# Kernel optimization log

Hardware: AMD Instinct MI355X
Metric: run time of the kernel (lower is better)

Reference implementation:

```python
import jax, jax.numpy as jnp
import numpy as np

CH = 512
GROUPS = 32
EPS = 1e-6


def setup_inputs() -> dict:
    key = jax.random.key(0)
    ks = jax.random.split(key, 12)
    b, c, h, w = 4, CH, 64, 64
    std = 1.0 / np.sqrt(c)
    return {
        "x": jax.random.normal(ks[0], (b, c, h, w), dtype=jnp.float32),
        "norm_gamma": jnp.ones((c,), jnp.float32),
        "norm_beta": jnp.zeros((c,), jnp.float32),
        "wq": jax.random.normal(ks[1], (c, c), jnp.float32) * std,
        "bq": jax.random.normal(ks[2], (c,), jnp.float32) * 0.01,
        "wk": jax.random.normal(ks[3], (c, c), jnp.float32) * std,
        "bk": jax.random.normal(ks[4], (c,), jnp.float32) * 0.01,
        "wv": jax.random.normal(ks[5], (c, c), jnp.float32) * std,
        "bv": jax.random.normal(ks[6], (c,), jnp.float32) * 0.01,
        "wo": jax.random.normal(ks[7], (c, c), jnp.float32) * std,
        "bo": jax.random.normal(ks[8], (c,), jnp.float32) * 0.01,
    }


def _group_norm(x, gamma, beta):
    b, c, h, w = x.shape
    xg = x.reshape(b, GROUPS, c // GROUPS, h, w)
    mean = xg.mean(axis=(2, 3, 4), keepdims=True)
    var = xg.var(axis=(2, 3, 4), keepdims=True)
    xn = ((xg - mean) * jax.lax.rsqrt(var + EPS)).reshape(b, c, h, w)
    return xn * gamma[None, :, None, None] + beta[None, :, None, None]


def reference(x, norm_gamma, norm_beta, wq, bq, wk, bk, wv, bv, wo, bo):
    b, c, h, w = x.shape
    hn = _group_norm(x, norm_gamma, norm_beta)
    hs = hn.reshape(b, c, h * w)  # [b, c, n]
    # 1x1 convs == per-pixel matmuls over channel dim (weight[out,in])
    q = jnp.einsum('oc,bcn->bno', wq, hs) + bq  # [b, n, c]
    k = jnp.einsum('oc,bcn->bon', wk, hs) + bk[None, :, None]  # [b, c, n]
    v = jnp.einsum('oc,bcn->bno', wv, hs) + bv  # [b, n, c]
    scale = c ** (-0.5)
    attn = jax.nn.softmax(jnp.einsum('bnc,bcm->bnm', q, k) * scale, axis=-1)
    out = jnp.einsum('bnm,bmc->bnc', attn, v)  # [b, n, c]
    out = jnp.einsum('oc,bnc->bon', wo, out) + bo[None, :, None]  # [b, c, n]
    return x + out.reshape(b, c, h, w)
```

## Files before the change

kernel.cpp:

```cpp
#include <hip/hip_runtime.h>
#include <hip/hip_bf16.h>
#include <cstdint>

typedef __bf16 bf16;
typedef __bf16 bf16x8 __attribute__((ext_vector_type(8)));
typedef __bf16 bf16x4 __attribute__((ext_vector_type(4)));
typedef float f32x4 __attribute__((ext_vector_type(4)));

__device__ __forceinline__ void gld_lds16(const void* g, void* l) {
  __builtin_amdgcn_global_load_lds((const __attribute__((address_space(1))) void*)g,
                                   (__attribute__((address_space(3))) void*)l, 16, 0, 0);
}

enum { BIAS_NONE = 0, BIAS_COL = 1, BIAS_ROW = 2, BIAS_QK = 3 };
enum { OUT_BF16 = 0, OUT_F32_RESID = 1 };

template<int BIAS_MODE, int OUT_MODE>
__global__ __launch_bounds__(256)
void gemm_bt(const bf16* __restrict__ A, long sA, int lda,
             const bf16* __restrict__ Bm, long sB, int ldb,
             void* __restrict__ Cv, long sC, int ldc,
             const float* __restrict__ bias, const float* __restrict__ bias2,
             const float* __restrict__ resid, long sR,
             int K, float scale)
{
  const int bm = blockIdx.x, bn = blockIdx.y, bz = blockIdx.z;
  const char* Ab = (const char*)(A + (long)bz * sA);
  const char* Bb = (const char*)(Bm + (long)bz * sB);
  const int tid = threadIdx.x;
  const int wave = tid >> 6, lane = tid & 63;
  const int wr = wave >> 1, wc = wave & 1;

  __shared__ __attribute__((aligned(128))) char lds[32768];
  char* ldsA = lds;
  char* ldsB = lds + 16384;

  uint32_t aoff[4], boff[4];
#pragma unroll
  for (int i = 0; i < 4; ++i) {
    uint32_t ra = (uint32_t)(wr * 64 + i * 16 + (lane & 15));
    uint32_t la = ra * 128u + (uint32_t)((lane >> 4) << 4);
    aoff[i] = la ^ ((la >> 3) & 0x70u);
    uint32_t rb = (uint32_t)(wc * 64 + i * 16 + (lane & 15));
    uint32_t lb = rb * 128u + (uint32_t)((lane >> 4) << 4);
    boff[i] = lb ^ ((lb >> 3) & 0x70u);
  }
  uint32_t srow[4], sinb[4];
#pragma unroll
  for (int t = 0; t < 4; ++t) {
    uint32_t paddr = (uint32_t)(((wave * 4 + t) * 64 + lane) * 16);
    uint32_t laddr = paddr ^ ((paddr >> 3) & 0x70u);
    srow[t] = laddr >> 7;
    sinb[t] = laddr & 127u;
  }

  const long ldab = (long)lda * 2, ldbb = (long)ldb * 2;
  const long arow0 = (long)bm * 128, brow0 = (long)bn * 128;
  f32x4 acc[4][4] = {};
  const int nK = K >> 6;
  for (int kt = 0; kt < nK; ++kt) {
    const long k0b = (long)kt * 128;
#pragma unroll
    for (int t = 0; t < 4; ++t) {
      gld_lds16(Ab + (arow0 + srow[t]) * ldab + k0b + sinb[t], ldsA + (wave * 4 + t) * 1024);
      gld_lds16(Bb + (brow0 + srow[t]) * ldbb + k0b + sinb[t], ldsB + (wave * 4 + t) * 1024);
    }
    __syncthreads();
#pragma unroll
    for (int kk = 0; kk < 2; ++kk) {
      bf16x8 af[4], bfr[4];
#pragma unroll
      for (int i = 0; i < 4; ++i) {
        af[i]  = *(const bf16x8*)(ldsA + (aoff[i] ^ (kk << 6)));
        bfr[i] = *(const bf16x8*)(ldsB + (boff[i] ^ (kk << 6)));
      }
#pragma unroll
      for (int mi = 0; mi < 4; ++mi)
#pragma unroll
        for (int ni = 0; ni < 4; ++ni)
          acc[mi][ni] = __builtin_amdgcn_mfma_f32_16x16x32_bf16(af[mi], bfr[ni], acc[mi][ni], 0, 0, 0);
    }
    __syncthreads();
  }

  const int cl = lane & 15, rq = lane >> 4;
  const long row0 = (long)bm * 128 + wr * 64;
  const long col0 = (long)bn * 128 + wc * 64;

  if constexpr (OUT_MODE == OUT_F32_RESID) {
    float* Co = (float*)Cv + (long)bz * sC;
    const float* X = resid + (long)bz * sR;
#pragma unroll
    for (int mi = 0; mi < 4; ++mi)
#pragma unroll
      for (int ni = 0; ni < 4; ++ni) {
        const long col = col0 + ni * 16 + cl;
#pragma unroll
        for (int j = 0; j < 4; ++j) {
          const long row = row0 + mi * 16 + rq * 4 + j;
          Co[row * ldc + col] = acc[mi][ni][j] + bias[row] + X[row * ldc + col];
        }
      }
  } else if constexpr (BIAS_MODE == BIAS_QK) {
    const bool isq = (col0 < 512);
    bf16* base = (bf16*)Cv + (long)bz * sC + (isq ? 0 : sR);
    const long csub = isq ? 0 : 512;
#pragma unroll
    for (int mi = 0; mi < 4; ++mi)
#pragma unroll
      for (int ni = 0; ni < 4; ++ni) {
        const long col = col0 + ni * 16 + cl;
        const float bc = isq ? bias[col] * scale : bias2[col - 512];
        const float vs = isq ? scale : 1.f;
#pragma unroll
        for (int j = 0; j < 4; ++j) {
          const long row = row0 + mi * 16 + rq * 4 + j;
          base[row * ldc + (col - csub)] = (bf16)(acc[mi][ni][j] * vs + bc);
        }
      }
  } else {
    bf16* Co = (bf16*)Cv + (long)bz * sC;
#pragma unroll
    for (int mi = 0; mi < 4; ++mi)
#pragma unroll
      for (int ni = 0; ni < 4; ++ni) {
        const long col = col0 + ni * 16 + cl;
        float bc = 0.f;
        if (BIAS_MODE == BIAS_COL) bc = bias[col] * scale;
#pragma unroll
        for (int j = 0; j < 4; ++j) {
          const long row = row0 + mi * 16 + rq * 4 + j;
          float v = acc[mi][ni][j] * (BIAS_MODE == BIAS_COL ? scale : 1.f) + bc;
          if (BIAS_MODE == BIAS_ROW) v += bias[row];
          Co[row * ldc + col] = (bf16)v;
        }
      }
  }
}

__global__ __launch_bounds__(256)
void sm_scan(const bf16* __restrict__ S, float2* __restrict__ rs)
{
  const long row = (long)blockIdx.x * 4 + (threadIdx.x >> 6);
  const int lane = threadIdx.x & 63;
  const bf16* p = S + row * 4096;
  float v[64];
#pragma unroll
  for (int i = 0; i < 8; ++i) {
    bf16x8 c = *(const bf16x8*)(p + (i * 64 + lane) * 8);
#pragma unroll
    for (int j = 0; j < 8; ++j) v[i * 8 + j] = (float)c[j];
  }
  float m = -3.0e38f;
#pragma unroll
  for (int i = 0; i < 64; ++i) m = fmaxf(m, v[i]);
#pragma unroll
  for (int d = 32; d > 0; d >>= 1) m = fmaxf(m, __shfl_xor(m, d, 64));
  float s = 0.f;
#pragma unroll
  for (int i = 0; i < 64; ++i) s += __expf(v[i] - m);
#pragma unroll
  for (int d = 32; d > 0; d >>= 1) s += __shfl_xor(s, d, 64);
  if (lane == 0) rs[row] = make_float2(m, 1.f / s);
}

__global__ __launch_bounds__(512, 2)
void gemm_pv2(const bf16* __restrict__ S, long sA,
              const bf16* __restrict__ Vm, long sB,
              bf16* __restrict__ O, long sC,
              const float2* __restrict__ rstat, long sRS, int swz)
{
  constexpr int T = 64;
  extern __shared__ char lds[];
  char* ldsA = lds;
  char* ldsB = lds + 16384;

  int bm, bz;
  if (swz) {
    const int bid = blockIdx.x;
    const int xcd = bid & 7;
    bz = xcd >> 1;
    bm = ((bid >> 3) << 1) | (xcd & 1);
  } else {
    bm = blockIdx.x; bz = blockIdx.z;
  }
  const char* Ab = (const char*)(S + (long)bz * sA) + (long)bm * 64 * 8192;
  const char* Bb = (const char*)(Vm + (long)bz * sB);
  const float2* rs = rstat + (long)bz * sRS;
  const int tid = threadIdx.x, wave = tid >> 6, lane = tid & 63;
  const int lg = lane >> 4, l15 = lane & 15;

  const uint32_t ar = (uint32_t)(tid >> 3), ab0 = (uint32_t)((tid & 7) * 16);
  const float Mr = rs[bm * 64 + ar].x;

  uint32_t bR[8], bIn[8];
#pragma unroll
  for (int j = 0; j < 8; ++j) {
    uint32_t s = (uint32_t)(j * 512 + tid);
    bR[j] = s >> 3;
    bIn[j] = (s & 7) * 16;
  }

  uint32_t aO[4], bO[4];
#pragma unroll
  for (int mi = 0; mi < 4; ++mi) {
    uint32_t r = (uint32_t)(mi * 16 + l15);
    aO[mi] = r * 128 + (((uint32_t)(lg * 16)) ^ ((r & 7) << 4));
  }
#pragma unroll
  for (int ni = 0; ni < 4; ++ni) {
    uint32_t r = (uint32_t)(wave * 64 + ni * 16 + l15);
    bO[ni] = r * 128 + (((uint32_t)(lg * 16)) ^ ((r & 7) << 4));
  }

  f32x4 acc[4][4] = {};

  auto stageB = [&](uint32_t nb, int t) {
#pragma unroll
    for (int j = 0; j < 8; ++j)
      gld_lds16(Bb + (long)bR[j] * 8192 + (long)t * 128 + (bIn[j] ^ ((bR[j] & 7) << 4)),
                ldsB + nb * 65536 + bR[j] * 128 + bIn[j]);
  };
  auto writeA = [&](uint32_t nb, bf16x8 sv) {
    bf16x8 pv;
#pragma unroll
    for (int j = 0; j < 8; ++j)
      pv[j] = (bf16)__expf((float)sv[j] - Mr);
    *(bf16x8*)(ldsA + nb * 8192 + ar * 128 + (ab0 ^ ((ar & 7) << 4))) = pv;
  };

  {
    bf16x8 sv0 = *(const bf16x8*)(Ab + (long)ar * 8192 + ab0);
    stageB(0, 0);
    writeA(0, sv0);
  }
  __syncthreads();

  for (int t = 0; t < T; ++t) {
    const uint32_t cur = (uint32_t)(t & 1), nxt = cur ^ 1u;
    bf16x8 svn;
    if (t + 1 < T) {
      svn = *(const bf16x8*)(Ab + (long)ar * 8192 + (long)(t + 1) * 128 + ab0);
      stageB(nxt, t + 1);
    }
    bf16x8 af[4][2], bfr[4][2];
#pragma unroll
    for (int mi = 0; mi < 4; ++mi)
#pragma unroll
      for (int kk = 0; kk < 2; ++kk)
        af[mi][kk] = *(const bf16x8*)(ldsA + ((cur * 8192 + aO[mi]) ^ (uint32_t)(kk << 6)));
#pragma unroll
    for (int ni = 0; ni < 4; ++ni)
#pragma unroll
      for (int kk = 0; kk < 2; ++kk)
        bfr[ni][kk] = *(const bf16x8*)(ldsB + ((cur * 65536 + bO[ni]) ^ (uint32_t)(kk << 6)));
#pragma unroll
    for (int mi = 0; mi < 4; ++mi)
#pragma unroll
      for (int ni = 0; ni < 4; ++ni)
#pragma unroll
        for (int kk = 0; kk < 2; ++kk)
          acc[mi][ni] = __builtin_amdgcn_mfma_f32_16x16x32_bf16(af[mi][kk], bfr[ni][kk], acc[mi][ni], 0, 0, 0);
    if (t + 1 < T) writeA(nxt, svn);
    __syncthreads();
  }

  bf16* Co = O + (long)bz * sC + (long)bm * 64 * 512;
#pragma unroll
  for (int mi = 0; mi < 4; ++mi)
#pragma unroll
    for (int j = 0; j < 4; ++j) {
      const int row = mi * 16 + lg * 4 + j;
      const float invL = rs[bm * 64 + row].y;
#pragma unroll
      for (int ni = 0; ni < 4; ++ni) {
        const int col = wave * 64 + ni * 16 + l15;
        Co[(long)row * 512 + col] = (bf16)(acc[mi][ni][j] * invL);
      }
    }
}

__global__ __launch_bounds__(256)
void gn_stats(const float* __restrict__ x, float* __restrict__ stats)
{
  const int bg = blockIdx.x;
  const float4* px = (const float4*)(x + (long)bg * 65536);
  float s1 = 0.f, s2 = 0.f;
  for (int i = threadIdx.x; i < 16384; i += 256) {
    float4 f = px[i];
    s1 += f.x + f.y + f.z + f.w;
    s2 += f.x * f.x + f.y * f.y + f.z * f.z + f.w * f.w;
  }
#pragma unroll
  for (int d = 32; d > 0; d >>= 1) {
    s1 += __shfl_xor(s1, d, 64);
    s2 += __shfl_xor(s2, d, 64);
  }
  __shared__ float r1[4], r2[4];
  const int wave = threadIdx.x >> 6, lane = threadIdx.x & 63;
  if (lane == 0) { r1[wave] = s1; r2[wave] = s2; }
  __syncthreads();
  if (threadIdx.x == 0) {
    float t1 = r1[0] + r1[1] + r1[2] + r1[3];
    float t2 = r2[0] + r2[1] + r2[2] + r2[3];
    float mean = t1 * (1.f / 65536.f);
    float var  = t2 * (1.f / 65536.f) - mean * mean;
    stats[bg * 2]     = mean;
    stats[bg * 2 + 1] = rsqrtf(var + 1e-6f);
  }
}

__global__ __launch_bounds__(256)
void gn_apply(const float* __restrict__ x, const float* __restrict__ stats,
              const float* __restrict__ gamma, const float* __restrict__ beta,
              bf16* __restrict__ hn)
{
  const int b = blockIdx.y;
  const int n0 = blockIdx.x * 64;
  __shared__ __attribute__((aligned(16))) char lt[65536];
  const int tid = threadIdx.x;
  for (int i = 0; i < 32; ++i) {
    int f = i * 256 + tid;
    int c = f >> 4;
    int n4 = f & 15;
    float4 xv = *(const float4*)(x + (((long)b * 512 + c) * 4096) + n0 + n4 * 4);
    int g = c >> 4;
    float mean = stats[(b * 32 + g) * 2];
    float rstd = stats[(b * 32 + g) * 2 + 1];
    float ga = gamma[c], be = beta[c];
    float y[4];
    y[0] = (xv.x - mean) * rstd * ga + be;
    y[1] = (xv.y - mean) * rstd * ga + be;
    y[2] = (xv.z - mean) * rstd * ga + be;
    y[3] = (xv.w - mean) * rstd * ga + be;
    uint32_t cb = (uint32_t)(c * 2);
#pragma unroll
    for (int jj = 0; jj < 4; ++jj) {
      uint32_t nl = (uint32_t)(n4 * 4 + jj);
      uint32_t phys = nl * 1024u + (cb ^ (((nl >> 2) & 7u) << 4));
      *(bf16*)(lt + phys) = (bf16)y[jj];
    }
  }
  __syncthreads();
  for (int i = 0; i < 16; ++i) {
    int j = i * 256 + tid;
    uint32_t row = (uint32_t)(j >> 6);
    uint32_t m = (uint32_t)(j & 63);
    uint32_t phys = row * 1024u + ((m * 16u) ^ (((row >> 2) & 7u) << 4));
    uint4 val = *(const uint4*)(lt + phys);
    *(uint4*)((char*)(hn + ((long)b * 4096 + n0 + row) * 512) + m * 16) = val;
  }
}

__global__ __launch_bounds__(256)
void conv_w4(const float* __restrict__ w0, const float* __restrict__ w1,
             const float* __restrict__ w2, const float* __restrict__ w3,
             bf16* __restrict__ dst)
{
  const int z = blockIdx.y;
  const float* src = (z == 0) ? w0 : (z == 1) ? w1 : (z == 2) ? w2 : w3;
  const int i = blockIdx.x * 256 + threadIdx.x;
  float4 f = ((const float4*)src)[i];
  bf16x4 o;
  o[0] = (bf16)f.x; o[1] = (bf16)f.y; o[2] = (bf16)f.z; o[3] = (bf16)f.w;
  ((bf16x4*)(dst))[(long)z * 65536 + i] = o;
}

extern "C" void kernel_launch(void* const* d_in, const int* in_sizes, int n_in,
                              void* d_out, int out_size, void* d_ws, size_t ws_size,
                              hipStream_t stream)
{
  const float* x     = (const float*)d_in[0];
  const float* gamma = (const float*)d_in[1];
  const float* beta  = (const float*)d_in[2];
  const float* wq = (const float*)d_in[3];
  const float* bq = (const float*)d_in[4];
  const float* wk = (const float*)d_in[5];
  const float* bk = (const float*)d_in[6];
  const float* wv = (const float*)d_in[7];
  const float* bv = (const float*)d_in[8];
  const float* wo = (const float*)d_in[9];
  const float* bo = (const float*)d_in[10];
  float* out = (float*)d_out;

  char* ws = (char*)d_ws;
  bf16* hn  = (bf16*)(ws + 0);
  bf16* q   = (bf16*)(ws + 16777216);
  bf16* k   = (bf16*)(ws + 33554432);
  bf16* v   = (bf16*)(ws + 50331648);
  bf16* O   = (bf16*)(ws + 67108864);
  bf16* wqb = (bf16*)(ws + 83886080);
  bf16* wvb = (bf16*)(ws + 84934656);
  bf16* wob = (bf16*)(ws + 85458944);
  float* gstats = (float*)(ws + 85983232);
  float2* rstat = (float2*)(ws + 85984256);
  bf16* S   = (bf16*)(ws + 86115328);

  const long sBC = 2097152;
  const long sS1 = 16777216;
  const long K_OFS = 8388608;
  const float scale = 0.044194173824159216f;

  const int LDS_PV = 147456;
  hipFuncSetAttribute(reinterpret_cast<const void*>(gemm_pv2),
                      hipFuncAttributeMaxDynamicSharedMemorySize, LDS_PV);

  conv_w4<<<dim3(256, 4), 256, 0, stream>>>(wq, wk, wv, wo, wqb);
  gn_stats<<<128, 256, 0, stream>>>(x, gstats);
  gn_apply<<<dim3(64, 4), 256, 0, stream>>>(x, gstats, gamma, beta, hn);

  gemm_bt<BIAS_QK, OUT_BF16><<<dim3(32, 8, 4), 256, 0, stream>>>(
      hn, sBC, 512, wqb, 0, 512, q, sBC, 512,
      bq, bk, nullptr, K_OFS, 512, scale);
  gemm_bt<BIAS_ROW, OUT_BF16><<<dim3(4, 32, 4), 256, 0, stream>>>(
      wvb, 0, 512, hn, sBC, 512, v, sBC, 4096,
      bv, nullptr, nullptr, 0, 512, 1.f);

  const bool tier1 = ws_size >= (size_t)220333056;
  if (tier1) {
    gemm_bt<BIAS_NONE, OUT_BF16><<<dim3(32, 32, 4), 256, 0, stream>>>(
        q, sBC, 512, k, sBC, 512, S, sS1, 4096,
        nullptr, nullptr, nullptr, 0, 512, 1.f);
    sm_scan<<<4096, 256, 0, stream>>>(S, (float2*)rstat);
    gemm_pv2<<<dim3(256, 1, 1), 512, LDS_PV, stream>>>(
        S, sS1, v, sBC, O, sBC, rstat, 4096, 1);
  } else {
    for (int b = 0; b < 4; ++b) {
      gemm_bt<BIAS_NONE, OUT_BF16><<<dim3(32, 32, 1), 256, 0, stream>>>(
          q + b * sBC, 0, 512, k + b * sBC, 0, 512, S, 0, 4096,
          nullptr, nullptr, nullptr, 0, 512, 1.f);
      sm_scan<<<1024, 256, 0, stream>>>(S, (float2*)rstat);
      gemm_pv2<<<dim3(64, 1, 1), 512, LDS_PV, stream>>>(
          S, 0, v + b * sBC, 0, O + b * sBC, 0, rstat, 0, 0);
    }
  }

  gemm_bt<BIAS_ROW, OUT_F32_RESID><<<dim3(4, 32, 4), 256, 0, stream>>>(
      wob, 0, 512, O, sBC, 512, out, sBC, 4096,
      bo, nullptr, x, sBC, 512, 1.f);
}
```

Before: 307.4 us.

## Deepen PV GEMM prefetch to two stages with manual waitcnt and barriers

Restructures the PV kernel's main loop to issue global loads two iterations ahead. The loop now uses explicit s_waitcnt vmcnt/lgkmcnt and raw s_barrier in place of __syncthreads, and raises wave priority around the MFMA block. The softmax-exp A tile is written to LDS before the barrier so async B loads can overlap the MFMAs. Launch bounds drop from 2 to 1 blocks per CU, and the hand-counted vmcnt values add correctness risk if the compiler emits a different number of memory ops.

```diff
diff --git a/kernel.cpp b/kernel.cpp
--- a/kernel.cpp
+++ b/kernel.cpp
@@ -164,8 +164,8 @@
   if (lane == 0) rs[row] = make_float2(m, 1.f / s);
 }
 
-__global__ __launch_bounds__(512, 2)
-void gemm_pv2(const bf16* __restrict__ S, long sA,
+__global__ __launch_bounds__(512, 1)
+void gemm_pv3(const bf16* __restrict__ S, long sA,
               const bf16* __restrict__ Vm, long sB,
               bf16* __restrict__ O, long sC,
               const float2* __restrict__ rstat, long sRS, int swz)
@@ -221,6 +221,9 @@
       gld_lds16(Bb + (long)bR[j] * 8192 + (long)t * 128 + (bIn[j] ^ ((bR[j] & 7) << 4)),
                 ldsB + nb * 65536 + bR[j] * 128 + bIn[j]);
   };
+  auto loadA = [&](int t) -> bf16x8 {
+    return *(const bf16x8*)(Ab + (long)ar * 8192 + (long)t * 128 + ab0);
+  };
   auto writeA = [&](uint32_t nb, bf16x8 sv) {
     bf16x8 pv;
 #pragma unroll
@@ -230,19 +233,20 @@
   };
 
   {
-    bf16x8 sv0 = *(const bf16x8*)(Ab + (long)ar * 8192 + ab0);
+    bf16x8 sv0 = loadA(0);
     stageB(0, 0);
     writeA(0, sv0);
   }
-  __syncthreads();
+  bf16x8 svn = loadA(1);
+  stageB(1, 1);
+  asm volatile("s_waitcnt vmcnt(9)" ::: "memory");
+  asm volatile("s_waitcnt lgkmcnt(0)" ::: "memory");
+  __builtin_amdgcn_sched_barrier(0);
+  __builtin_amdgcn_s_barrier();
 
   for (int t = 0; t < T; ++t) {
     const uint32_t cur = (uint32_t)(t & 1), nxt = cur ^ 1u;
-    bf16x8 svn;
-    if (t + 1 < T) {
-      svn = *(const bf16x8*)(Ab + (long)ar * 8192 + (long)(t + 1) * 128 + ab0);
-      stageB(nxt, t + 1);
-    }
+
     bf16x8 af[4][2], bfr[4][2];
 #pragma unroll
     for (int mi = 0; mi < 4; ++mi)
@@ -254,6 +258,19 @@
 #pragma unroll
       for (int kk = 0; kk < 2; ++kk)
         bfr[ni][kk] = *(const bf16x8*)(ldsB + ((cur * 65536 + bO[ni]) ^ (uint32_t)(kk << 6)));
+
+    if (t + 1 < T) writeA(nxt, svn);
+
+    asm volatile("s_waitcnt lgkmcnt(0)" ::: "memory");
+    __builtin_amdgcn_sched_barrier(0);
+    __builtin_amdgcn_s_barrier();
+
+    if (t + 2 < T) {
+      svn = loadA(t + 2);
+      stageB(cur, t + 2);
+    }
+
+    __builtin_amdgcn_s_setprio(1);
 #pragma unroll
     for (int mi = 0; mi < 4; ++mi)
 #pragma unroll
@@ -261,8 +278,13 @@
 #pragma unroll
         for (int kk = 0; kk < 2; ++kk)
           acc[mi][ni] = __builtin_amdgcn_mfma_f32_16x16x32_bf16(af[mi][kk], bfr[ni][kk], acc[mi][ni], 0, 0, 0);
-    if (t + 1 < T) writeA(nxt, svn);
-    __syncthreads();
+    __builtin_amdgcn_s_setprio(0);
+
+    if (t + 1 < T) {
+      if (t + 2 < T) asm volatile("s_waitcnt vmcnt(9)" ::: "memory");
+      else           asm volatile("s_waitcnt vmcnt(0)" ::: "memory");
+      __builtin_amdgcn_s_barrier();
+    }
   }
 
   bf16* Co = O + (long)bz * sC + (long)bm * 64 * 512;
@@ -402,7 +424,7 @@
   const float scale = 0.044194173824159216f;
 
   const int LDS_PV = 147456;
-  hipFuncSetAttribute(reinterpret_cast<const void*>(gemm_pv2),
+  hipFuncSetAttribute(reinterpret_cast<const void*>(gemm_pv3),
                       hipFuncAttributeMaxDynamicSharedMemorySize, LDS_PV);
 
   conv_w4<<<dim3(256, 4), 256, 0, stream>>>(wq, wk, wv, wo, wqb);
@@ -422,7 +444,7 @@
         q, sBC, 512, k, sBC, 512, S, sS1, 4096,
         nullptr, nullptr, nullptr, 0, 512, 1.f);
     sm_scan<<<4096, 256, 0, stream>>>(S, (float2*)rstat);
-    gemm_pv2<<<dim3(256, 1, 1), 512, LDS_PV, stream>>>(
+    gemm_pv3<<<dim3(256, 1, 1), 512, LDS_PV, stream>>>(
         S, sS1, v, sBC, O, sBC, rstat, 4096, 1);
   } else {
     for (int b = 0; b < 4; ++b) {
@@ -430,7 +452,7 @@
           q + b * sBC, 0, 512, k + b * sBC, 0, 512, S, 0, 4096,
           nullptr, nullptr, nullptr, 0, 512, 1.f);
       sm_scan<<<1024, 256, 0, stream>>>(S, (float2*)rstat);
-      gemm_pv2<<<dim3(64, 1, 1), 512, LDS_PV, stream>>>(
+      gemm_pv3<<<dim3(64, 1, 1), 512, LDS_PV, stream>>>(
           S, 0, v + b * sBC, 0, O + b * sBC, 0, rstat, 0, 0);
     }
   }
```

New measurement: 299.3 us. 1.03x faster.
